# Kernel optimization log

Hardware: AMD Instinct MI355X
Metric: run time of the kernel (lower is better)

Reference implementation:

```python
import jax, jax.numpy as jnp
import numpy as np

B, T_Q, T_C = 4, 2048, 2048
Q_DIM = C_DIM = H_DIM = OUT_DIM = 1024
N_HEADS = 16
D = H_DIM // N_HEADS


def setup_inputs() -> dict:
    key = jax.random.key(0)
    ks = jax.random.split(key, 10)
    s_q = 1.0 / np.sqrt(Q_DIM)
    s_c = 1.0 / np.sqrt(C_DIM)
    s_h = 1.0 / np.sqrt(H_DIM)
    return {
        "query": jax.random.normal(ks[0], (B, T_Q, Q_DIM), jnp.float32),
        "context": jax.random.normal(ks[1], (B, T_C, C_DIM), jnp.float32),
        "Wq": jax.random.uniform(ks[2], (Q_DIM, H_DIM), jnp.float32, -s_q, s_q),
        "bq": jax.random.uniform(ks[3], (H_DIM,), jnp.float32, -s_q, s_q),
        "Wk": jax.random.uniform(ks[4], (C_DIM, H_DIM), jnp.float32, -s_c, s_c),
        "bk": jax.random.uniform(ks[5], (H_DIM,), jnp.float32, -s_c, s_c),
        "Wv": jax.random.uniform(ks[6], (C_DIM, H_DIM), jnp.float32, -s_c, s_c),
        "bv": jax.random.uniform(ks[7], (H_DIM,), jnp.float32, -s_c, s_c),
        "Wo": jax.random.uniform(ks[8], (H_DIM, OUT_DIM), jnp.float32, -s_h, s_h),
        "bo": jax.random.uniform(ks[9], (OUT_DIM,), jnp.float32, -s_h, s_h),
    }


def reference(query, context, Wq, bq, Wk, bk, Wv, bv, Wo, bo):
    Bq, Tq, _ = query.shape
    _, Tc, _ = context.shape
    # project and split heads: [B, H, T, D]
    q = (query @ Wq + bq).reshape(Bq, Tq, N_HEADS, D).transpose(0, 2, 1, 3)
    k = (context @ Wk + bk).reshape(Bq, Tc, N_HEADS, D).transpose(0, 2, 1, 3)
    v = (context @ Wv + bv).reshape(Bq, Tc, N_HEADS, D).transpose(0, 2, 1, 3)
    scores = jnp.einsum("bhqd,bhkd->bhqk", q, k) / jnp.sqrt(jnp.float32(D))
    probs = jax.nn.softmax(scores, axis=-1)
    attn = jnp.einsum("bhqk,bhkd->bhqd", probs, v)  # dropout p=0 -> identity
    attn = attn.transpose(0, 2, 1, 3).reshape(Bq, Tq, N_HEADS * D)
    return attn @ Wo + bo
```

## Files before the change

kernel.cpp:

```cpp
#include <hip/hip_runtime.h>
#include <hip/hip_bf16.h>
#include <cstdint>

typedef __attribute__((ext_vector_type(8))) short short8;
typedef __attribute__((ext_vector_type(4))) short short4_t;
typedef __attribute__((ext_vector_type(4))) float f32x4;

#define MFMA16(a, b, c) __builtin_amdgcn_mfma_f32_16x16x32_bf16(a, b, c, 0, 0, 0)

__device__ __forceinline__ short f2b(float f) {
    union { float fp; unsigned u; } un; un.fp = f;
    unsigned r = un.u + 0x7fffu + ((un.u >> 16) & 1u);
    return (short)(r >> 16);
}

__device__ __forceinline__ unsigned pk_bf16(float a, float b) {
    unsigned r;
    asm("v_cvt_pk_bf16_f32 %0, %1, %2" : "=v"(r) : "v"(a), "v"(b));
    return r;
}

union pk8_u { unsigned u4[4]; short8 s8; };
union pk4_u { unsigned u2[2]; short4_t s4; };
union cat8_u { short4_t s4[2]; short8 s8; };

typedef const __attribute__((address_space(1))) unsigned g_as1;
typedef __attribute__((address_space(3))) unsigned l_as3;
__device__ __forceinline__ void gll16(const ushort* g, ushort* l) {
    __builtin_amdgcn_global_load_lds((g_as1*)g, (l_as3*)l, 16, 0, 0);
}

__global__ __launch_bounds__(256) void cvt_all_kernel(
    const float* __restrict__ q, const float* __restrict__ c,
    ushort* __restrict__ qb, ushort* __restrict__ cb,
    const float* __restrict__ Wq, const float* __restrict__ Wk,
    const float* __restrict__ Wv, const float* __restrict__ Wo,
    ushort* __restrict__ wt)
{
    __shared__ float Ts[64 * 65];
    const int id = blockIdx.x;
    const int tid = threadIdx.x;

    if (id < 8192) {
        const float* src = (id >= 4096) ? c : q;
        ushort* dst = (id >= 4096) ? cb : qb;
        size_t i = ((size_t)(id & 4095) * 256 + tid) * 8;
        float4 v0 = *(const float4*)&src[i];
        float4 v1 = *(const float4*)&src[i + 4];
        uint4 o;
        o.x = pk_bf16(v0.x, v0.y); o.y = pk_bf16(v0.z, v0.w);
        o.z = pk_bf16(v1.x, v1.y); o.w = pk_bf16(v1.z, v1.w);
        *(uint4*)&dst[i] = o;
        return;
    }

    const int u = id - 8192;
    const int z = u >> 8;
    const float* W = (z == 0) ? Wq : (z == 1) ? Wk : (z == 2) ? Wv : Wo;
    ushort* WT = wt + (size_t)z * (1024 * 1024);
    const int n0 = (u & 15) * 64, k0 = ((u >> 4) & 15) * 64;

#pragma unroll
    for (int rr = 0; rr < 4; ++rr) {
        int uu = tid + rr * 256;
        int r = uu >> 4, cc = (uu & 15) * 4;
        float4 v = *(const float4*)&W[(size_t)(k0 + r) * 1024 + n0 + cc];
        Ts[r * 65 + cc + 0] = v.x; Ts[r * 65 + cc + 1] = v.y;
        Ts[r * 65 + cc + 2] = v.z; Ts[r * 65 + cc + 3] = v.w;
    }
    __syncthreads();
#pragma unroll
    for (int rr = 0; rr < 4; ++rr) {
        int uu = tid + rr * 256;
        int rn = uu >> 4, ck = (uu & 15) * 4;
        pk4_u o;
        o.u2[0] = pk_bf16(Ts[(ck + 0) * 65 + rn], Ts[(ck + 1) * 65 + rn]);
        o.u2[1] = pk_bf16(Ts[(ck + 2) * 65 + rn], Ts[(ck + 3) * 65 + rn]);
        *(short4_t*)&WT[(size_t)(n0 + rn) * 1024 + k0 + ck] = o.s4;
    }
}

__global__ __launch_bounds__(256) void proj_kernel(
    const ushort* __restrict__ Qb, const ushort* __restrict__ Cb,
    const ushort* __restrict__ WTbase,
    const float* __restrict__ biasq, const float* __restrict__ biask,
    const float* __restrict__ biasv,
    ushort* __restrict__ Qw, ushort* __restrict__ Kw, ushort* __restrict__ Vtw,
    float scale)
{
    __shared__ ushort As[128 * 64];
    __shared__ ushort Bs[128 * 64];
    const int tid = threadIdx.x;
    const int w = tid >> 6, lane = tid & 63;
    const int ln = tid & 15, quad = (tid >> 4) & 3;
    const int wm = w >> 1, wn = w & 1;

    const int hw = blockIdx.x;
    const int lid = (hw & 7) * 192 + (hw >> 3);
    const int mode = lid >> 9;
    const int rem = lid & 511;
    const int m0 = (rem >> 3) * 128;
    const int n0 = (rem & 7) * 128;
    const ushort* Ag = (mode == 2) ? Qb : Cb;
    const ushort* BT = (mode == 2) ? WTbase : WTbase + (size_t)(1 + mode) * 1048576;

    int offA[4], offB[4], lseg[4];
#pragma unroll
    for (int rr = 0; rr < 4; ++rr) {
        int idx = (rr * 4 + w) * 64 + lane;
        int r = idx >> 3, cst = idx & 7, csrc = cst ^ (r & 7);
        offA[rr] = (m0 + r) * 1024 + csrc * 8;
        offB[rr] = (n0 + r) * 1024 + csrc * 8;
        lseg[rr] = (rr * 4 + w) * 512;
    }

    f32x4 acc[4][4] = {};

    for (int kk = 0; kk < 1024; kk += 64) {
        __syncthreads();
#pragma unroll
        for (int rr = 0; rr < 4; ++rr)
            gll16(&Ag[(size_t)(offA[rr] + kk)], &As[lseg[rr]]);
#pragma unroll
        for (int rr = 0; rr < 4; ++rr)
            gll16(&BT[(size_t)(offB[rr] + kk)], &Bs[lseg[rr]]);
        __syncthreads();

#pragma unroll
        for (int ks = 0; ks < 2; ++ks) {
            short8 af[4], bfr[4];
#pragma unroll
            for (int i = 0; i < 4; ++i)
                af[i] = *(const short8*)&As[(wm * 64 + i * 16 + ln) * 64 +
                                            ((ks * 4 + quad) ^ (ln & 7)) * 8];
#pragma unroll
            for (int j = 0; j < 4; ++j)
                bfr[j] = *(const short8*)&Bs[(wn * 64 + j * 16 + ln) * 64 +
                                             ((ks * 4 + quad) ^ (ln & 7)) * 8];
#pragma unroll
            for (int i = 0; i < 4; ++i)
#pragma unroll
                for (int j = 0; j < 4; ++j)
                    acc[i][j] = MFMA16(af[i], bfr[j], acc[i][j]);
        }
    }

    if (mode == 1) {
#pragma unroll
        for (int j = 0; j < 4; ++j) {
            int n = n0 + wn * 64 + j * 16 + ln;
            int h = n >> 6, d = n & 63;
            float bvv = biasv[n];
#pragma unroll
            for (int i = 0; i < 4; ++i) {
                int mb = m0 + wm * 64 + i * 16 + quad * 4;
                int b = mb >> 11, t = mb & 2047;
                pk4_u o;
                o.u2[0] = pk_bf16(acc[i][j][0] + bvv, acc[i][j][1] + bvv);
                o.u2[1] = pk_bf16(acc[i][j][2] + bvv, acc[i][j][3] + bvv);
                *(short4_t*)&Vtw[(((size_t)((b * 16 + h) * 64 + d)) << 11) + t] = o.s4;
            }
        }
    } else {
        ushort* Out = (mode == 2) ? Qw : Kw;
        const float* bias = (mode == 2) ? biasq : biask;
        float sc = (mode == 2) ? scale : 1.0f;
#pragma unroll
        for (int j = 0; j < 4; ++j) {
            int n = n0 + wn * 64 + j * 16 + ln;
            int h = n >> 6, d = n & 63;
            float bvv = bias[n];
#pragma unroll
            for (int i = 0; i < 4; ++i) {
                int mb = m0 + wm * 64 + i * 16 + quad * 4;
#pragma unroll
                for (int r = 0; r < 4; ++r) {
                    int m = mb + r, b = m >> 11, t = m & 2047;
                    Out[(((size_t)(b * 16 + h) * 2048 + t) << 6) + d] =
                        (ushort)f2b((acc[i][j][r] + bvv) * sc);
                }
            }
        }
    }
}

__global__ __launch_bounds__(256) void gemm_o_kernel(
    const ushort* __restrict__ Ag, const ushort* __restrict__ BT,
    const float* __restrict__ bias, float* __restrict__ Out)
{
    __shared__ ushort As[128 * 64];
    __shared__ ushort Bs[128 * 64];
    const int tid = threadIdx.x;
    const int w = tid >> 6, lane = tid & 63;
    const int ln = tid & 15, quad = (tid >> 4) & 3;
    const int wm = w >> 1, wn = w & 1;
    const int hw = blockIdx.x;
    const int lid = (hw & 7) * 64 + (hw >> 3);
    const int m0 = (lid >> 3) * 128, n0 = (lid & 7) * 128;

    int offA[4], offB[4], lseg[4];
#pragma unroll
    for (int rr = 0; rr < 4; ++rr) {
        int idx = (rr * 4 + w) * 64 + lane;
        int r = idx >> 3, cst = idx & 7, csrc = cst ^ (r & 7);
        offA[rr] = (m0 + r) * 1024 + csrc * 8;
        offB[rr] = (n0 + r) * 1024 + csrc * 8;
        lseg[rr] = (rr * 4 + w) * 512;
    }

    f32x4 acc[4][4] = {};

    for (int kk = 0; kk < 1024; kk += 64) {
        __syncthreads();
#pragma unroll
        for (int rr = 0; rr < 4; ++rr)
            gll16(&Ag[(size_t)(offA[rr] + kk)], &As[lseg[rr]]);
#pragma unroll
        for (int rr = 0; rr < 4; ++rr)
            gll16(&BT[(size_t)(offB[rr] + kk)], &Bs[lseg[rr]]);
        __syncthreads();

#pragma unroll
        for (int ks = 0; ks < 2; ++ks) {
            short8 af[4], bfr[4];
#pragma unroll
            for (int i = 0; i < 4; ++i)
                af[i] = *(const short8*)&As[(wm * 64 + i * 16 + ln) * 64 +
                                            ((ks * 4 + quad) ^ (ln & 7)) * 8];
#pragma unroll
            for (int j = 0; j < 4; ++j)
                bfr[j] = *(const short8*)&Bs[(wn * 64 + j * 16 + ln) * 64 +
                                             ((ks * 4 + quad) ^ (ln & 7)) * 8];
#pragma unroll
            for (int i = 0; i < 4; ++i)
#pragma unroll
                for (int j = 0; j < 4; ++j)
                    acc[i][j] = MFMA16(af[i], bfr[j], acc[i][j]);
        }
    }

#pragma unroll
    for (int j = 0; j < 4; ++j) {
        int n = n0 + wn * 64 + j * 16 + ln;
        float bv = bias[n];
#pragma unroll
        for (int i = 0; i < 4; ++i) {
            int mb = m0 + wm * 64 + i * 16 + quad * 4;
#pragma unroll
            for (int r = 0; r < 4; ++r)
                Out[(size_t)(mb + r) * 1024 + n] = acc[i][j][r] + bv;
        }
    }
}

__global__ __launch_bounds__(256, 4) void attn_kernel(
    const ushort* __restrict__ Qw, const ushort* __restrict__ Kw,
    const ushort* __restrict__ Vtw, ushort* __restrict__ attn)
{
    __shared__ ushort Ks[2][4096];
    __shared__ ushort Vts[2][4096];

    const int tid = threadIdx.x;
    const int w = tid >> 6, lane = tid & 63;
    const int ln = tid & 15, quad = (tid >> 4) & 3;
    const int id = blockIdx.x;
    const int qt = (id >> 3) & 15;
    const int bh = (id & 7) | ((id >> 7) << 3);
    const int b = bh >> 4, h = bh & 15;

    const ushort* Qg = Qw + (size_t)bh * 131072 + (size_t)qt * 8192;
    const ushort* Kg = Kw + (size_t)bh * 131072;
    const ushort* Vg = Vtw + (size_t)bh * 131072;

    short8 bq[2][2];
#pragma unroll
    for (int qs = 0; qs < 2; ++qs)
#pragma unroll
        for (int ks = 0; ks < 2; ++ks)
            bq[qs][ks] = *(const short8*)&Qg[(w * 32 + qs * 16 + ln) * 64 + ks * 32 + quad * 8];

    int offK[2], offV[2], lseg[2];
#pragma unroll
    for (int rr = 0; rr < 2; ++rr) {
        int idx = (rr * 4 + w) * 64 + lane;
        int r = idx >> 3, cst = idx & 7, csrc = cst ^ (r & 7);
        offK[rr] = r * 64 + csrc * 8;
        offV[rr] = r * 2048 + csrc * 8;
        lseg[rr] = (rr * 4 + w) * 512;
    }

    const short8 ones8 = {(short)0x3F80, (short)0x3F80, (short)0x3F80, (short)0x3F80,
                          (short)0x3F80, (short)0x3F80, (short)0x3F80, (short)0x3F80};

    f32x4 Of[2][4] = {};
    f32x4 lac[2] = {};

#pragma unroll
    for (int rr = 0; rr < 2; ++rr) gll16(&Kg[offK[rr]], &Ks[0][lseg[rr]]);
#pragma unroll
    for (int rr = 0; rr < 2; ++rr) gll16(&Vg[offV[rr]], &Vts[0][lseg[rr]]);
    __syncthreads();

    auto body = [&](int kt, const ushort* Kc, const ushort* Vc,
                    ushort* Kn, ushort* Vn) {
        if (kt < 31) {
#pragma unroll
            for (int rr = 0; rr < 2; ++rr)
                gll16(&Kg[(kt + 1) * 4096 + offK[rr]], &Kn[lseg[rr]]);
#pragma unroll
            for (int rr = 0; rr < 2; ++rr)
                gll16(&Vg[(kt + 1) * 64 + offV[rr]], &Vn[lseg[rr]]);
        }

#pragma unroll
        for (int c = 0; c < 2; ++c) {
            short8 a0[2], a1[2];
#pragma unroll
            for (int kb = 0; kb < 2; ++kb) {
                int kv = 2 * c + kb;
                a0[kb] = *(const short8*)&Kc[(kv * 16 + ln) * 64 + (quad ^ (ln & 7)) * 8];
                a1[kb] = *(const short8*)&Kc[(kv * 16 + ln) * 64 + ((4 + quad) ^ (ln & 7)) * 8];
            }
            f32x4 s[2][2];
            __builtin_amdgcn_s_setprio(1);
#pragma unroll
            for (int kb = 0; kb < 2; ++kb)
#pragma unroll
                for (int qs = 0; qs < 2; ++qs) {
                    f32x4 t = {};
                    t = MFMA16(a0[kb], bq[qs][0], t);
                    t = MFMA16(a1[kb], bq[qs][1], t);
                    s[kb][qs] = t;
                }
            __builtin_amdgcn_s_setprio(0);

            short8 pf8[2];
#pragma unroll
            for (int qs = 0; qs < 2; ++qs) {
                pk8_u pu;
                pu.u4[0] = pk_bf16(__builtin_amdgcn_exp2f(s[0][qs][0]),
                                   __builtin_amdgcn_exp2f(s[0][qs][1]));
                pu.u4[1] = pk_bf16(__builtin_amdgcn_exp2f(s[0][qs][2]),
                                   __builtin_amdgcn_exp2f(s[0][qs][3]));
                pu.u4[2] = pk_bf16(__builtin_amdgcn_exp2f(s[1][qs][0]),
                                   __builtin_amdgcn_exp2f(s[1][qs][1]));
                pu.u4[3] = pk_bf16(__builtin_amdgcn_exp2f(s[1][qs][2]),
                                   __builtin_amdgcn_exp2f(s[1][qs][3]));
                pf8[qs] = pu.s8;
                lac[qs] = MFMA16(ones8, pu.s8, lac[qs]);
            }

            cat8_u av[4];
#pragma unroll
            for (int ds = 0; ds < 4; ++ds) {
                const ushort* vrow = &Vc[(ds * 16 + ln) * 64];
                av[ds].s4[0] = *(const short4_t*)&vrow[(((4 * c + (quad >> 1)) ^ (ln & 7)) * 8) + (quad & 1) * 4];
                av[ds].s4[1] = *(const short4_t*)&vrow[(((4 * c + 2 + (quad >> 1)) ^ (ln & 7)) * 8) + (quad & 1) * 4];
            }
            __builtin_amdgcn_s_setprio(1);
#pragma unroll
            for (int ds = 0; ds < 4; ++ds)
#pragma unroll
                for (int qs = 0; qs < 2; ++qs)
                    Of[qs][ds] = MFMA16(av[ds].s8, pf8[qs], Of[qs][ds]);
            __builtin_amdgcn_s_setprio(0);
        }

        __syncthreads();
    };

    for (int kt = 0; kt < 32; kt += 2) {
        body(kt,     Ks[0], Vts[0], Ks[1], Vts[1]);
        body(kt + 1, Ks[1], Vts[1], Ks[0], Vts[0]);
    }

#pragma unroll
    for (int qs = 0; qs < 2; ++qs) {
        float inv = __builtin_amdgcn_rcpf(lac[qs][0]);
        int t = qt * 128 + w * 32 + qs * 16 + ln;
        size_t base = ((size_t)(b * 2048 + t) << 10) + h * 64;
#pragma unroll
        for (int ds = 0; ds < 4; ++ds) {
            uint2 o;
            o.x = pk_bf16(Of[qs][ds][0] * inv, Of[qs][ds][1] * inv);
            o.y = pk_bf16(Of[qs][ds][2] * inv, Of[qs][ds][3] * inv);
            *(uint2*)&attn[base + ds * 16 + quad * 4] = o;
        }
    }
}

extern "C" void kernel_launch(void* const* d_in, const int* in_sizes, int n_in,
                              void* d_out, int out_size, void* d_ws, size_t ws_size,
                              hipStream_t stream)
{
    const float* query   = (const float*)d_in[0];
    const float* context = (const float*)d_in[1];
    const float* Wq = (const float*)d_in[2];
    const float* bq = (const float*)d_in[3];
    const float* Wk = (const float*)d_in[4];
    const float* bk = (const float*)d_in[5];
    const float* Wv = (const float*)d_in[6];
    const float* bv = (const float*)d_in[7];
    const float* Wo = (const float*)d_in[8];
    const float* bo = (const float*)d_in[9];

    char* ws = (char*)d_ws;
    ushort* WT  = (ushort*)ws;
    ushort* Qb  = (ushort*)(ws + 8388608);
    ushort* Qw  = (ushort*)(ws + 25165824);
    ushort* Kw  = (ushort*)(ws + 41943040);
    ushort* Vtw = (ushort*)(ws + 58720256);
    ushort* Aw  = Qb;
    ushort* Cb  = (ushort*)d_out;

    const float SCALE = 0.18033688011112042f;

    cvt_all_kernel<<<dim3(9216), 256, 0, stream>>>(query, context, Qb, Cb,
                                                   Wq, Wk, Wv, Wo, WT);
    proj_kernel<<<dim3(1536), 256, 0, stream>>>(Qb, Cb, WT, bq, bk, bv,
                                                Qw, Kw, Vtw, SCALE);
    attn_kernel<<<dim3(1024), 256, 0, stream>>>(Qw, Kw, Vtw, Aw);
    gemm_o_kernel<<<dim3(512), 256, 0, stream>>>(Aw, WT + 3 * 1048576, bo,
                                                 (float*)d_out);
}
```

Baseline: 296.2 us.

## Fuse K and V projections into one block sharing the context tile

The projection kernel now computes K and V together in a single block: the context A-tile is loaded once and multiplied against both Wk and Wv, with two accumulator sets. The grid shrinks from 1536 to 1024 blocks, where the first 512 (per XCD ordering) do K+V and the rest do Q. This halves context tile loads for K/V. In exchange it doubles LDS for B and the accumulator registers, which lowers occupancy, and the blocks become imbalanced because K/V blocks do twice the MFMA work of Q blocks.

```diff
diff --git a/kernel.cpp b/kernel.cpp
--- a/kernel.cpp
+++ b/kernel.cpp
@@ -89,32 +89,34 @@
     float scale)
 {
     __shared__ ushort As[128 * 64];
-    __shared__ ushort Bs[128 * 64];
+    __shared__ ushort Bs0[128 * 64];
+    __shared__ ushort Bs1[128 * 64];
     const int tid = threadIdx.x;
     const int w = tid >> 6, lane = tid & 63;
     const int ln = tid & 15, quad = (tid >> 4) & 3;
     const int wm = w >> 1, wn = w & 1;
 
     const int hw = blockIdx.x;
-    const int lid = (hw & 7) * 192 + (hw >> 3);
-    const int mode = lid >> 9;
-    const int rem = lid & 511;
-    const int m0 = (rem >> 3) * 128;
-    const int n0 = (rem & 7) * 128;
-    const ushort* Ag = (mode == 2) ? Qb : Cb;
-    const ushort* BT = (mode == 2) ? WTbase : WTbase + (size_t)(1 + mode) * 1048576;
+    const int xcd = hw & 7, ord = hw >> 3;
+    const bool kv = (ord < 64);
+    const int idx = xcd * 64 + (kv ? ord : ord - 64);
+    const int m0 = (idx >> 3) * 128, n0 = (idx & 7) * 128;
+    const ushort* Ag = kv ? Cb : Qb;
+    const ushort* BT0 = kv ? (WTbase + 1048576) : WTbase;
+    const ushort* BT1 = WTbase + 2 * 1048576;
 
     int offA[4], offB[4], lseg[4];
 #pragma unroll
     for (int rr = 0; rr < 4; ++rr) {
-        int idx = (rr * 4 + w) * 64 + lane;
-        int r = idx >> 3, cst = idx & 7, csrc = cst ^ (r & 7);
+        int idx2 = (rr * 4 + w) * 64 + lane;
+        int r = idx2 >> 3, cst = idx2 & 7, csrc = cst ^ (r & 7);
         offA[rr] = (m0 + r) * 1024 + csrc * 8;
         offB[rr] = (n0 + r) * 1024 + csrc * 8;
         lseg[rr] = (rr * 4 + w) * 512;
     }
 
-    f32x4 acc[4][4] = {};
+    f32x4 acck[4][4] = {};
+    f32x4 accv[4][4] = {};
 
     for (int kk = 0; kk < 1024; kk += 64) {
         __syncthreads();
@@ -123,7 +125,12 @@
             gll16(&Ag[(size_t)(offA[rr] + kk)], &As[lseg[rr]]);
 #pragma unroll
         for (int rr = 0; rr < 4; ++rr)
-            gll16(&BT[(size_t)(offB[rr] + kk)], &Bs[lseg[rr]]);
+            gll16(&BT0[(size_t)(offB[rr] + kk)], &Bs0[lseg[rr]]);
+        if (kv) {
+#pragma unroll
+            for (int rr = 0; rr < 4; ++rr)
+                gll16(&BT1[(size_t)(offB[rr] + kk)], &Bs1[lseg[rr]]);
+        }
         __syncthreads();
 
 #pragma unroll
@@ -135,49 +142,63 @@
                                             ((ks * 4 + quad) ^ (ln & 7)) * 8];
 #pragma unroll
             for (int j = 0; j < 4; ++j)
-                bfr[j] = *(const short8*)&Bs[(wn * 64 + j * 16 + ln) * 64 +
-                                             ((ks * 4 + quad) ^ (ln & 7)) * 8];
+                bfr[j] = *(const short8*)&Bs0[(wn * 64 + j * 16 + ln) * 64 +
+                                              ((ks * 4 + quad) ^ (ln & 7)) * 8];
 #pragma unroll
             for (int i = 0; i < 4; ++i)
 #pragma unroll
                 for (int j = 0; j < 4; ++j)
-                    acc[i][j] = MFMA16(af[i], bfr[j], acc[i][j]);
-        }
-    }
-
-    if (mode == 1) {
+                    acck[i][j] = MFMA16(af[i], bfr[j], acck[i][j]);
+            if (kv) {
+#pragma unroll
+                for (int j = 0; j < 4; ++j)
+                    bfr[j] = *(const short8*)&Bs1[(wn * 64 + j * 16 + ln) * 64 +
+                                                  ((ks * 4 + quad) ^ (ln & 7)) * 8];
+#pragma unroll
+                for (int i = 0; i < 4; ++i)
+#pragma unroll
+                    for (int j = 0; j < 4; ++j)
+                        accv[i][j] = MFMA16(af[i], bfr[j], accv[i][j]);
+            }
+        }
+    }
+
+    if (kv) {
 #pragma unroll
         for (int j = 0; j < 4; ++j) {
             int n = n0 + wn * 64 + j * 16 + ln;
             int h = n >> 6, d = n & 63;
-            float bvv = biasv[n];
+            float bkk = biask[n], bvv = biasv[n];
 #pragma unroll
             for (int i = 0; i < 4; ++i) {
                 int mb = m0 + wm * 64 + i * 16 + quad * 4;
-                int b = mb >> 11, t = mb & 2047;
+#pragma unroll
+                for (int r = 0; r < 4; ++r) {
+                    int m = mb + r, b = m >> 11, t = m & 2047;
+                    Kw[(((size_t)(b * 16 + h) * 2048 + t) << 6) + d] =
+                        (ushort)f2b(acck[i][j][r] + bkk);
+                }
+                int b2 = mb >> 11, t2 = mb & 2047;
                 pk4_u o;
-                o.u2[0] = pk_bf16(acc[i][j][0] + bvv, acc[i][j][1] + bvv);
-                o.u2[1] = pk_bf16(acc[i][j][2] + bvv, acc[i][j][3] + bvv);
-                *(short4_t*)&Vtw[(((size_t)((b * 16 + h) * 64 + d)) << 11) + t] = o.s4;
+                o.u2[0] = pk_bf16(accv[i][j][0] + bvv, accv[i][j][1] + bvv);
+                o.u2[1] = pk_bf16(accv[i][j][2] + bvv, accv[i][j][3] + bvv);
+                *(short4_t*)&Vtw[(((size_t)((b2 * 16 + h) * 64 + d)) << 11) + t2] = o.s4;
             }
         }
     } else {
-        ushort* Out = (mode == 2) ? Qw : Kw;
-        const float* bias = (mode == 2) ? biasq : biask;
-        float sc = (mode == 2) ? scale : 1.0f;
 #pragma unroll
         for (int j = 0; j < 4; ++j) {
             int n = n0 + wn * 64 + j * 16 + ln;
             int h = n >> 6, d = n & 63;
-            float bvv = bias[n];
+            float bvv = biasq[n];
 #pragma unroll
             for (int i = 0; i < 4; ++i) {
                 int mb = m0 + wm * 64 + i * 16 + quad * 4;
 #pragma unroll
                 for (int r = 0; r < 4; ++r) {
                     int m = mb + r, b = m >> 11, t = m & 2047;
-                    Out[(((size_t)(b * 16 + h) * 2048 + t) << 6) + d] =
-                        (ushort)f2b((acc[i][j][r] + bvv) * sc);
+                    Qw[(((size_t)(b * 16 + h) * 2048 + t) << 6) + d] =
+                        (ushort)f2b((acck[i][j][r] + bvv) * scale);
                 }
             }
         }
@@ -417,7 +438,7 @@
 
     cvt_all_kernel<<<dim3(9216), 256, 0, stream>>>(query, context, Qb, Cb,
                                                    Wq, Wk, Wv, Wo, WT);
-    proj_kernel<<<dim3(1536), 256, 0, stream>>>(Qb, Cb, WT, bq, bk, bv,
+    proj_kernel<<<dim3(1024), 256, 0, stream>>>(Qb, Cb, WT, bq, bk, bv,
                                                 Qw, Kw, Vtw, SCALE);
     attn_kernel<<<dim3(1024), 256, 0, stream>>>(Qw, Kw, Vtw, Aw);
     gemm_o_kernel<<<dim3(512), 256, 0, stream>>>(Aw, WT + 3 * 1048576, bo,
```

After: 313.6 us. +5.9%, slower.

## Double-buffer A tile in LDS and read B fragments directly from global

Applied to the files above, without the earlier changes.

In both the projection and output GEMM kernels, the A operand tile is now double-buffered in shared memory so the next K-slice load is issued before computing on the current one, with one barrier per iteration instead of two. The B (weight) operand is no longer staged through LDS; each lane loads its MFMA fragments straight from global memory, relying on cache reuse across blocks. This removes half the LDS traffic and a barrier, but exposes global-load latency on the B path with no prefetch, and each B element is fetched by both wm wave rows.

```diff
diff --git a/kernel.cpp b/kernel.cpp
--- a/kernel.cpp
+++ b/kernel.cpp
@@ -88,8 +88,7 @@
     ushort* __restrict__ Qw, ushort* __restrict__ Kw, ushort* __restrict__ Vtw,
     float scale)
 {
-    __shared__ ushort As[128 * 64];
-    __shared__ ushort Bs[128 * 64];
+    __shared__ ushort As[2][128 * 64];
     const int tid = threadIdx.x;
     const int w = tid >> 6, lane = tid & 63;
     const int ln = tid & 15, quad = (tid >> 4) & 3;
@@ -104,45 +103,49 @@
     const ushort* Ag = (mode == 2) ? Qb : Cb;
     const ushort* BT = (mode == 2) ? WTbase : WTbase + (size_t)(1 + mode) * 1048576;
 
-    int offA[4], offB[4], lseg[4];
+    int offA[4], lseg[4];
 #pragma unroll
     for (int rr = 0; rr < 4; ++rr) {
-        int idx = (rr * 4 + w) * 64 + lane;
-        int r = idx >> 3, cst = idx & 7, csrc = cst ^ (r & 7);
+        int idx2 = (rr * 4 + w) * 64 + lane;
+        int r = idx2 >> 3, cst = idx2 & 7, csrc = cst ^ (r & 7);
         offA[rr] = (m0 + r) * 1024 + csrc * 8;
-        offB[rr] = (n0 + r) * 1024 + csrc * 8;
         lseg[rr] = (rr * 4 + w) * 512;
     }
+    const ushort* Bp = BT + (size_t)(n0 + wn * 64 + ln) * 1024;
 
     f32x4 acc[4][4] = {};
 
-    for (int kk = 0; kk < 1024; kk += 64) {
-        __syncthreads();
-#pragma unroll
-        for (int rr = 0; rr < 4; ++rr)
-            gll16(&Ag[(size_t)(offA[rr] + kk)], &As[lseg[rr]]);
-#pragma unroll
-        for (int rr = 0; rr < 4; ++rr)
-            gll16(&BT[(size_t)(offB[rr] + kk)], &Bs[lseg[rr]]);
-        __syncthreads();
-
+#pragma unroll
+    for (int rr = 0; rr < 4; ++rr)
+        gll16(&Ag[(size_t)offA[rr]], &As[0][lseg[rr]]);
+    __syncthreads();
+
+    for (int kt = 0; kt < 16; ++kt) {
+        const int cur = kt & 1;
+        if (kt < 15) {
+#pragma unroll
+            for (int rr = 0; rr < 4; ++rr)
+                gll16(&Ag[(size_t)(offA[rr] + (kt + 1) * 64)], &As[cur ^ 1][lseg[rr]]);
+        }
+        const ushort* Ac = As[cur];
 #pragma unroll
         for (int ks = 0; ks < 2; ++ks) {
             short8 af[4], bfr[4];
 #pragma unroll
             for (int i = 0; i < 4; ++i)
-                af[i] = *(const short8*)&As[(wm * 64 + i * 16 + ln) * 64 +
+                af[i] = *(const short8*)&Ac[(wm * 64 + i * 16 + ln) * 64 +
                                             ((ks * 4 + quad) ^ (ln & 7)) * 8];
 #pragma unroll
             for (int j = 0; j < 4; ++j)
-                bfr[j] = *(const short8*)&Bs[(wn * 64 + j * 16 + ln) * 64 +
-                                             ((ks * 4 + quad) ^ (ln & 7)) * 8];
+                bfr[j] = *(const short8*)&Bp[(size_t)(j * 16) * 1024 +
+                                             kt * 64 + (ks * 4 + quad) * 8];
 #pragma unroll
             for (int i = 0; i < 4; ++i)
 #pragma unroll
                 for (int j = 0; j < 4; ++j)
                     acc[i][j] = MFMA16(af[i], bfr[j], acc[i][j]);
         }
+        __syncthreads();
     }
 
     if (mode == 1) {
@@ -188,8 +191,7 @@
     const ushort* __restrict__ Ag, const ushort* __restrict__ BT,
     const float* __restrict__ bias, float* __restrict__ Out)
 {
-    __shared__ ushort As[128 * 64];
-    __shared__ ushort Bs[128 * 64];
+    __shared__ ushort As[2][128 * 64];
     const int tid = threadIdx.x;
     const int w = tid >> 6, lane = tid & 63;
     const int ln = tid & 15, quad = (tid >> 4) & 3;
@@ -198,45 +200,49 @@
     const int lid = (hw & 7) * 64 + (hw >> 3);
     const int m0 = (lid >> 3) * 128, n0 = (lid & 7) * 128;
 
-    int offA[4], offB[4], lseg[4];
+    int offA[4], lseg[4];
 #pragma unroll
     for (int rr = 0; rr < 4; ++rr) {
         int idx = (rr * 4 + w) * 64 + lane;
         int r = idx >> 3, cst = idx & 7, csrc = cst ^ (r & 7);
         offA[rr] = (m0 + r) * 1024 + csrc * 8;
-        offB[rr] = (n0 + r) * 1024 + csrc * 8;
         lseg[rr] = (rr * 4 + w) * 512;
     }
+    const ushort* Bp = BT + (size_t)(n0 + wn * 64 + ln) * 1024;
 
     f32x4 acc[4][4] = {};
 
-    for (int kk = 0; kk < 1024; kk += 64) {
-        __syncthreads();
-#pragma unroll
-        for (int rr = 0; rr < 4; ++rr)
-            gll16(&Ag[(size_t)(offA[rr] + kk)], &As[lseg[rr]]);
-#pragma unroll
-        for (int rr = 0; rr < 4; ++rr)
-            gll16(&BT[(size_t)(offB[rr] + kk)], &Bs[lseg[rr]]);
-        __syncthreads();
-
+#pragma unroll
+    for (int rr = 0; rr < 4; ++rr)
+        gll16(&Ag[(size_t)offA[rr]], &As[0][lseg[rr]]);
+    __syncthreads();
+
+    for (int kt = 0; kt < 16; ++kt) {
+        const int cur = kt & 1;
+        if (kt < 15) {
+#pragma unroll
+            for (int rr = 0; rr < 4; ++rr)
+                gll16(&Ag[(size_t)(offA[rr] + (kt + 1) * 64)], &As[cur ^ 1][lseg[rr]]);
+        }
+        const ushort* Ac = As[cur];
 #pragma unroll
         for (int ks = 0; ks < 2; ++ks) {
             short8 af[4], bfr[4];
 #pragma unroll
             for (int i = 0; i < 4; ++i)
-                af[i] = *(const short8*)&As[(wm * 64 + i * 16 + ln) * 64 +
+                af[i] = *(const short8*)&Ac[(wm * 64 + i * 16 + ln) * 64 +
                                             ((ks * 4 + quad) ^ (ln & 7)) * 8];
 #pragma unroll
             for (int j = 0; j < 4; ++j)
-                bfr[j] = *(const short8*)&Bs[(wn * 64 + j * 16 + ln) * 64 +
-                                             ((ks * 4 + quad) ^ (ln & 7)) * 8];
+                bfr[j] = *(const short8*)&Bp[(size_t)(j * 16) * 1024 +
+                                             kt * 64 + (ks * 4 + quad) * 8];
 #pragma unroll
             for (int i = 0; i < 4; ++i)
 #pragma unroll
                 for (int j = 0; j < 4; ++j)
                     acc[i][j] = MFMA16(af[i], bfr[j], acc[i][j]);
         }
+        __syncthreads();
     }
 
 #pragma unroll
```

Result: slower. 349.8 us (+18.1%).
